# Kernel optimization log

Measured on AMD Instinct MI355X. Metric: run time of the kernel, lower is better.

Reference implementation:

```python
import jax, jax.numpy as jnp
import numpy as np

B = 1024          # batch
H = W = 64        # image height/width
WIN = 2           # patch window (non-overlapping 2x2)
N = (H // WIN) * (W // WIN)   # 1024 DNPU nodes
N_ELEC = 7        # electrodes per DNPU device
N_IN = 4
N_CTRL = 3        # control electrodes per node
HID = 90          # surrogate MLP hidden width
OUT = 32          # out_size (OUT*OUT == N)


def setup_inputs() -> dict:
    key = jax.random.key(0)
    ks = jax.random.split(key, 8)
    x = jax.random.normal(ks[0], (B, 1, H, W), jnp.float32)
    # learned control voltages per node, in a typical DNPU voltage range
    controls = jax.random.uniform(ks[1], (N, N_CTRL), jnp.float32, -1.2, 0.6)
    # per-node electrode assignment: random permutation of the 7 electrodes;
    # first 4 are data-input electrodes, last 3 are control electrodes
    perms = jax.vmap(lambda k: jax.random.permutation(k, N_ELEC))(
        jax.random.split(ks[2], N))
    inputs_list = perms[:, :N_IN].astype(jnp.int32)
    control_list = perms[:, N_IN:].astype(jnp.int32)
    # shared surrogate-model MLP (7 -> 90 -> 90 -> 1)
    W1 = jax.random.normal(ks[3], (N_ELEC, HID), jnp.float32) * 0.3
    b1 = jax.random.normal(ks[4], (HID,), jnp.float32) * 0.1
    W2 = jax.random.normal(ks[5], (HID, HID), jnp.float32) * 0.1
    b2 = jax.random.normal(ks[6], (HID,), jnp.float32) * 0.1
    W3 = jax.random.normal(ks[7], (HID, 1), jnp.float32) * 0.1
    b3 = jnp.zeros((1,), jnp.float32)
    return {"x": x, "controls": controls, "W1": W1, "b1": b1,
            "W2": W2, "b2": b2, "W3": W3, "b3": b3,
            "inputs_list": inputs_list, "control_list": control_list}


def reference(x, controls, W1, b1, W2, b2, W3, b3, inputs_list, control_list):
    Bx = x.shape[0]
    # nf.unfold(x, kernel_size=2, stride=2): element order (c, kh, kw),
    # blocks row-major over spatial positions -> [B, 4, N]
    p = x.reshape(Bx, 1, H // WIN, WIN, W // WIN, WIN)
    p = p.transpose(0, 1, 3, 5, 2, 4).reshape(Bx, WIN * WIN, N)
    patches = p.transpose(0, 2, 1)                       # [B, N, 4]
    # assemble the 7-electrode input per node (vectorized scatter over nodes)
    node = jnp.arange(N)[:, None]
    E = jnp.zeros((Bx, N, N_ELEC), x.dtype)
    E = E.at[:, node, inputs_list].set(patches)          # data electrodes
    E = E.at[:, node, control_list].set(
        jnp.broadcast_to(controls, (Bx, N, N_CTRL)))     # control electrodes
    # shared surrogate MLP applied to every (batch, node) electrode vector
    h = jax.nn.elu(jnp.einsum('bne,eh->bnh', E, W1) + b1)  # [B, N, 90]
    h = jax.nn.elu(h @ W2 + b2)                            # [B, N, 90]
    out = (h @ W3 + b3)[..., 0]                            # [B, N] (concat over nodes)
    return out.reshape(-1, OUT, OUT)                       # out_size view
```

## Files before the change

kernel.cpp:

```cpp
#include <hip/hip_runtime.h>
#include <stdint.h>


#define HID 90

typedef float  f32x4 __attribute__((ext_vector_type(4)));
typedef _Float16 f16x8 __attribute__((ext_vector_type(8)));

#define WS_W1P 0
#define WS_B2V 720
#define WS_W3V 816
#define WS_B3  912
#define WS_W2F 928
#define WS_TOT_ELEMS (928 + 9216)

__global__ void prep_kernel(const float* __restrict__ W1, const float* __restrict__ b1,
                            const float* __restrict__ W2, const float* __restrict__ b2,
                            const float* __restrict__ W3, const float* __restrict__ b3,
                            float* __restrict__ wsf)
{
    _Float16* w2f = (_Float16*)(wsf + WS_W2F);
    for (int i = blockIdx.x * blockDim.x + threadIdx.x; i < WS_TOT_ELEMS;
         i += gridDim.x * blockDim.x) {
        if (i < 928) {
            float v = 0.f;
            if (i < WS_B2V) {
                const int k = i >> 3, e = i & 7;
                v = (e < 7) ? W1[e * HID + k] : b1[k];
            } else if (i < WS_W3V) {
                const int j = i - WS_B2V; v = (j < HID) ? b2[j] : 0.f;
            } else if (i < WS_B3) {
                const int j = i - WS_W3V; v = (j < HID) ? W3[j] : 0.f;
            } else if (i == WS_B3) {
                v = b3[0];
            }
            wsf[i] = v;
        } else {
            const int e  = i - 928;
            const int f  = e >> 9;
            const int r  = e & 511;
            const int l  = r >> 3, ii = r & 7;
            const int ks = f / 6, jt = f - ks * 6;
            const int k  = ks * 32 + ((l >> 4) << 3) + ii;
            const int j  = jt * 16 + (l & 15);
            const float v = (k < HID && j < HID) ? W2[k * HID + j] : 0.f;
            w2f[e] = (_Float16)v;
        }
    }
}

__device__ __forceinline__ float elu_f(float x) {
    return fmaxf(x, 0.f) + (__expf(fminf(x, 0.f)) - 1.f);
}

__device__ __forceinline__ uint32_t pk_f16(float a, float b) {
    auto r = __builtin_amdgcn_cvt_pkrtz(a, b);
    return __builtin_bit_cast(uint32_t, r);
}

__global__ __launch_bounds__(256, 2)
void dnpu_main(const float* __restrict__ x,
               const float* __restrict__ controls,
               const int* __restrict__ inputs_list,
               const int* __restrict__ control_list,
               const float* __restrict__ wsf,
               float* __restrict__ out)
{
    __shared__ alignas(16) _Float16 Hs[4 * 3 * 4 * 64 * 8];

    const int t    = threadIdx.x;
    const int row  = blockIdx.x * 256 + t;
    const int b    = row >> 10;
    const int n    = row & 1023;
    const int ph   = n >> 5, pw = n & 31;
    const int w    = t >> 6;
    const int lane = t & 63;
    const int rt_w = lane >> 4;
    const int lj   = lane & 15;

    const float* xp = x + ((size_t)b << 12) + (ph * 2) * 64 + pw * 2;
    const float2 pA = *(const float2*)xp;
    const float2 pB = *(const float2*)(xp + 64);

    const int4 il  = *(const int4*)(inputs_list + (n << 2));
    const int  cl0 = control_list[n * 3 + 0];
    const int  cl1 = control_list[n * 3 + 1];
    const int  cl2 = control_list[n * 3 + 2];
    const float c0 = controls[n * 3 + 0];
    const float c1 = controls[n * 3 + 1];
    const float c2 = controls[n * 3 + 2];

    float E[8];
    E[7] = 1.0f;
#pragma unroll
    for (int e = 0; e < 7; ++e) {
        float v = 0.f;
        v = (il.x == e) ? pA.x : v;
        v = (il.y == e) ? pA.y : v;
        v = (il.z == e) ? pB.x : v;
        v = (il.w == e) ? pB.y : v;
        v = (cl0 == e) ? c0 : v;
        v = (cl1 == e) ? c1 : v;
        v = (cl2 == e) ? c2 : v;
        E[e] = v;
    }

    const float* W1P = wsf + WS_W1P;
#pragma unroll
    for (int ks = 0; ks < 3; ++ks) {
#pragma unroll
        for (int lg = 0; lg < 4; ++lg) {
            uint32_t pk4[4];
#pragma unroll
            for (int p = 0; p < 4; ++p) {
                const int k = ks * 32 + lg * 8 + p * 2;
                if (k < HID) {
                    const float* wA = W1P + (k << 3);
                    float pa0 = 0.f, pa1 = 0.f, pb0 = 0.f, pb1 = 0.f;
#pragma unroll
                    for (int e = 0; e < 8; e += 2) {
                        pa0 = __builtin_fmaf(E[e],     wA[e],     pa0);
                        pa1 = __builtin_fmaf(E[e + 1], wA[e + 1], pa1);
                        pb0 = __builtin_fmaf(E[e],     wA[e + 8], pb0);
                        pb1 = __builtin_fmaf(E[e + 1], wA[e + 9], pb1);
                    }
                    pk4[p] = pk_f16(elu_f(pa0 + pa1), elu_f(pb0 + pb1));
                } else {
                    pk4[p] = 0u;
                }
            }
            const int slot = ((w * 3 + ks) * 4 + rt_w) * 64 + lg * 16 + lj;
            uint4 v4; v4.x = pk4[0]; v4.y = pk4[1]; v4.z = pk4[2]; v4.w = pk4[3];
            *(uint4*)&Hs[slot * 8] = v4;
        }
    }

    const float* B2V = wsf + WS_B2V;
    const float* W3V = wsf + WS_W3V;
    float b2j[6], w3j[6];
#pragma unroll
    for (int jt = 0; jt < 6; ++jt) {
        b2j[jt] = B2V[jt * 16 + lj];
        w3j[jt] = W3V[jt * 16 + lj];
    }
    const float B3v = wsf[WS_B3];

    f32x4 acc[4][6];
#pragma unroll
    for (int rt = 0; rt < 4; ++rt)
#pragma unroll
        for (int jt = 0; jt < 6; ++jt)
            acc[rt][jt] = (f32x4){b2j[jt], b2j[jt], b2j[jt], b2j[jt]};


    const _Float16* w2f = (const _Float16*)(wsf + WS_W2F);
#pragma unroll
    for (int ks = 0; ks < 3; ++ks) {
        f16x8 bfr[6];
#pragma unroll
        for (int jt = 0; jt < 6; ++jt)
            bfr[jt] = *(const f16x8*)(w2f + (((ks * 6 + jt) * 64 + lane) << 3));
        f16x8 afr[4];
#pragma unroll
        for (int rt = 0; rt < 4; ++rt)
            afr[rt] = *(const f16x8*)&Hs[(((w * 3 + ks) * 4 + rt) * 64 + lane) * 8];
#pragma unroll
        for (int rt = 0; rt < 4; ++rt)
#pragma unroll
            for (int jt = 0; jt < 6; ++jt)
                acc[rt][jt] = __builtin_amdgcn_mfma_f32_16x16x32_f16(
                    afr[rt], bfr[jt], acc[rt][jt], 0, 0, 0);
    }

    const int lg = lane >> 4;
    const int rowbase = blockIdx.x * 256 + w * 64;
#pragma unroll
    for (int rt = 0; rt < 4; ++rt) {
        float p0 = 0.f, p1 = 0.f, p2 = 0.f, p3 = 0.f;
#pragma unroll
        for (int jt = 0; jt < 6; ++jt) {
            p0 += elu_f(acc[rt][jt][0]) * w3j[jt];
            p1 += elu_f(acc[rt][jt][1]) * w3j[jt];
            p2 += elu_f(acc[rt][jt][2]) * w3j[jt];
            p3 += elu_f(acc[rt][jt][3]) * w3j[jt];
        }
#pragma unroll
        for (int mask = 1; mask < 16; mask <<= 1) {
            p0 += __shfl_xor(p0, mask);
            p1 += __shfl_xor(p1, mask);
            p2 += __shfl_xor(p2, mask);
            p3 += __shfl_xor(p3, mask);
        }
        if (lj < 4) {
            const float v = (lj == 0) ? p0 : (lj == 1) ? p1 : (lj == 2) ? p2 : p3;
            out[rowbase + rt * 16 + 4 * lg + lj] = v + B3v;
        }
    }
}

extern "C" void kernel_launch(void* const* d_in, const int* in_sizes, int n_in,
                              void* d_out, int out_size, void* d_ws, size_t ws_size,
                              hipStream_t stream)
{
    const float* x          = (const float*)d_in[0];
    const float* controls   = (const float*)d_in[1];
    const float* W1         = (const float*)d_in[2];
    const float* b1         = (const float*)d_in[3];
    const float* W2         = (const float*)d_in[4];
    const float* b2         = (const float*)d_in[5];
    const float* W3         = (const float*)d_in[6];
    const float* b3         = (const float*)d_in[7];
    const int* inputs_list  = (const int*)d_in[8];
    const int* control_list = (const int*)d_in[9];
    float* out = (float*)d_out;
    float* wsf = (float*)d_ws;

    hipLaunchKernelGGL(prep_kernel, dim3(40), dim3(256), 0, stream,
                       W1, b1, W2, b2, W3, b3, wsf);
    hipLaunchKernelGGL(dnpu_main, dim3(4096), dim3(256), 0, stream,
                       x, controls, inputs_list, control_list, wsf, out);
}
```

Measured before the change: 166.1 us.

## Cut registers and LDS: loop MFMA over output tiles, reuse smaller LDS buffer

The second-layer MFMA loop is reordered so the output-column tile is outermost, keeping only 4 accumulators live instead of 24. The ELU and W3 dot product are folded into that loop. The H staging buffer in LDS shrinks to one k-slice per wave, and the A fragments are read back into registers after each slice, so the buffer is reused. Launch bounds rise to 4 blocks per SM to raise occupancy. The trade-off is reloading B fragments per tile and holding 12 A fragments in registers. Reusing LDS within a wave also relies on wave-level ordering with no barrier.

```diff
diff --git a/kernel.cpp b/kernel.cpp
--- a/kernel.cpp
+++ b/kernel.cpp
@@ -58,7 +58,7 @@
     return __builtin_bit_cast(uint32_t, r);
 }
 
-__global__ __launch_bounds__(256, 2)
+__global__ __launch_bounds__(256, 4)
 void dnpu_main(const float* __restrict__ x,
                const float* __restrict__ controls,
                const int* __restrict__ inputs_list,
@@ -66,7 +66,7 @@
                const float* __restrict__ wsf,
                float* __restrict__ out)
 {
-    __shared__ alignas(16) _Float16 Hs[4 * 3 * 4 * 64 * 8];
+    __shared__ alignas(16) _Float16 Hs[4 * 4 * 64 * 8];
 
     const int t    = threadIdx.x;
     const int row  = blockIdx.x * 256 + t;
@@ -106,6 +106,7 @@
     }
 
     const float* W1P = wsf + WS_W1P;
+    uint4 af[3][4];
 #pragma unroll
     for (int ks = 0; ks < 3; ++ks) {
 #pragma unroll
@@ -129,10 +130,13 @@
                     pk4[p] = 0u;
                 }
             }
-            const int slot = ((w * 3 + ks) * 4 + rt_w) * 64 + lg * 16 + lj;
+            const int slot = (w * 4 + rt_w) * 64 + lg * 16 + lj;
             uint4 v4; v4.x = pk4[0]; v4.y = pk4[1]; v4.z = pk4[2]; v4.w = pk4[3];
             *(uint4*)&Hs[slot * 8] = v4;
         }
+#pragma unroll
+        for (int rt = 0; rt < 4; ++rt)
+            af[ks][rt] = *(const uint4*)&Hs[((w * 4 + rt) * 64 + lane) * 8];
     }
 
     const float* B2V = wsf + WS_B2V;
@@ -145,45 +149,40 @@
     }
     const float B3v = wsf[WS_B3];
 
-    f32x4 acc[4][6];
-#pragma unroll
-    for (int rt = 0; rt < 4; ++rt)
-#pragma unroll
-        for (int jt = 0; jt < 6; ++jt)
-            acc[rt][jt] = (f32x4){b2j[jt], b2j[jt], b2j[jt], b2j[jt]};
-
-
     const _Float16* w2f = (const _Float16*)(wsf + WS_W2F);
-#pragma unroll
-    for (int ks = 0; ks < 3; ++ks) {
-        f16x8 bfr[6];
-#pragma unroll
-        for (int jt = 0; jt < 6; ++jt)
-            bfr[jt] = *(const f16x8*)(w2f + (((ks * 6 + jt) * 64 + lane) << 3));
-        f16x8 afr[4];
+    f32x4 psum[4];
+#pragma unroll
+    for (int rt = 0; rt < 4; ++rt) psum[rt] = (f32x4){0.f, 0.f, 0.f, 0.f};
+
+#pragma unroll
+    for (int jt = 0; jt < 6; ++jt) {
+        f32x4 acc[4];
 #pragma unroll
         for (int rt = 0; rt < 4; ++rt)
-            afr[rt] = *(const f16x8*)&Hs[(((w * 3 + ks) * 4 + rt) * 64 + lane) * 8];
-#pragma unroll
-        for (int rt = 0; rt < 4; ++rt)
-#pragma unroll
-            for (int jt = 0; jt < 6; ++jt)
-                acc[rt][jt] = __builtin_amdgcn_mfma_f32_16x16x32_f16(
-                    afr[rt], bfr[jt], acc[rt][jt], 0, 0, 0);
+            acc[rt] = (f32x4){b2j[jt], b2j[jt], b2j[jt], b2j[jt]};
+#pragma unroll
+        for (int ks = 0; ks < 3; ++ks) {
+            const f16x8 bfr = *(const f16x8*)(w2f + (((ks * 6 + jt) * 64 + lane) << 3));
+#pragma unroll
+            for (int rt = 0; rt < 4; ++rt)
+                acc[rt] = __builtin_amdgcn_mfma_f32_16x16x32_f16(
+                    __builtin_bit_cast(f16x8, af[ks][rt]), bfr, acc[rt], 0, 0, 0);
+        }
+        const float w3 = w3j[jt];
+#pragma unroll
+        for (int rt = 0; rt < 4; ++rt) {
+            psum[rt][0] = __builtin_fmaf(elu_f(acc[rt][0]), w3, psum[rt][0]);
+            psum[rt][1] = __builtin_fmaf(elu_f(acc[rt][1]), w3, psum[rt][1]);
+            psum[rt][2] = __builtin_fmaf(elu_f(acc[rt][2]), w3, psum[rt][2]);
+            psum[rt][3] = __builtin_fmaf(elu_f(acc[rt][3]), w3, psum[rt][3]);
+        }
     }
 
     const int lg = lane >> 4;
     const int rowbase = blockIdx.x * 256 + w * 64;
 #pragma unroll
     for (int rt = 0; rt < 4; ++rt) {
-        float p0 = 0.f, p1 = 0.f, p2 = 0.f, p3 = 0.f;
-#pragma unroll
-        for (int jt = 0; jt < 6; ++jt) {
-            p0 += elu_f(acc[rt][jt][0]) * w3j[jt];
-            p1 += elu_f(acc[rt][jt][1]) * w3j[jt];
-            p2 += elu_f(acc[rt][jt][2]) * w3j[jt];
-            p3 += elu_f(acc[rt][jt][3]) * w3j[jt];
-        }
+        float p0 = psum[rt][0], p1 = psum[rt][1], p2 = psum[rt][2], p3 = psum[rt][3];
 #pragma unroll
         for (int mask = 1; mask < 16; mask <<= 1) {
             p0 += __shfl_xor(p0, mask);
```

Measured after the change: 159.6 us. 3.9% less time.
